# Optimization experiments

Measured on AMD Instinct MI355X. Metric: run time of the kernel, lower is better.

The kernel has to match this reference:

```python
import jax, jax.numpy as jnp
import numpy as np

N_NODES = 50000
N_EDGES = 800000
IN_SIZE, HID_SIZE, OUT_SIZE = 512, 128, 64


def _graph_conv(feat, src, dst, W, b, out_norm, in_norm, activation=None):
    # DGL GraphConv with norm='both': h' = D_in^{-1/2} A D_out^{-1/2} (X W) + b
    x = feat * out_norm[:, None]          # scale by source (out-degree) norm
    x = x @ W                             # dense transform first (in >= out)
    msg = x[src]                          # gather per-edge messages [E, d]
    agg = jax.ops.segment_sum(msg, dst, num_segments=N_NODES)
    h = agg * in_norm[:, None] + b
    if activation is not None:
        h = activation(h)
    return h


def setup_inputs() -> dict:
    key = jax.random.key(0)
    k1, k2, k3, k4, k5, k6, k7 = jax.random.split(key, 7)
    features = jax.random.normal(k1, (N_NODES, IN_SIZE), dtype=jnp.float32)
    src = jax.random.randint(k2, (N_EDGES,), 0, N_NODES, dtype=jnp.int64)
    dst = jax.random.randint(k3, (N_EDGES,), 0, N_NODES, dtype=jnp.int64)
    # Glorot-style init as in dglnn.GraphConv
    W1 = jax.random.normal(k4, (IN_SIZE, HID_SIZE), dtype=jnp.float32) * (1.0 / np.sqrt(IN_SIZE))
    b1 = jnp.zeros((HID_SIZE,), dtype=jnp.float32)
    W2 = jax.random.normal(k5, (HID_SIZE, OUT_SIZE), dtype=jnp.float32) * (1.0 / np.sqrt(HID_SIZE))
    b2 = jnp.zeros((OUT_SIZE,), dtype=jnp.float32)
    return {"features": features, "W1": W1, "b1": b1, "W2": W2, "b2": b2,
            "src": src, "dst": dst}


def reference(features, W1, b1, W2, b2, src, dst):
    ones = jnp.ones((N_EDGES,), dtype=features.dtype)
    out_deg = jax.ops.segment_sum(ones, src, num_segments=N_NODES)
    in_deg = jax.ops.segment_sum(ones, dst, num_segments=N_NODES)
    out_norm = jax.lax.rsqrt(jnp.clip(out_deg, 1.0))  # deg clamped to >=1 as in DGL
    in_norm = jax.lax.rsqrt(jnp.clip(in_deg, 1.0))
    h = _graph_conv(features, src, dst, W1, b1, out_norm, in_norm, activation=jax.nn.relu)
    # dropout omitted (eval mode)
    h = _graph_conv(h, src, dst, W2, b2, out_norm, in_norm, activation=None)
    return h
```

## Files before the change

### kernel.cpp

```cpp
#include <hip/hip_runtime.h>

#define N_NODES 50000
#define IN_SIZE 512
#define HID 128
#define OUT 64
#define NB 256
#define SHIFT 7
#define NBUCK 391
#define SB 64
#define NBINS32 25000

typedef _Float16 f16x8 __attribute__((ext_vector_type(8)));
typedef _Float16 f16x2 __attribute__((ext_vector_type(2)));
typedef float    f32x4 __attribute__((ext_vector_type(4)));

__device__ __forceinline__ bool detect_w(const int* p, int t, int* sh) {
    if (t < 64) {
        unsigned long long m = __ballot(p[2 * t + 1] == 0);
        if (t == 0) *sh = (m == ~0ull) ? 1 : 0;
    }
    __syncthreads();
    return *sh != 0;
}

__device__ __forceinline__ int load_idx(const void* p, int e, bool w) {
    return w ? (int)((const long long*)p)[e] : ((const int*)p)[e];
}

__global__ __launch_bounds__(256) void k_chist_wt(const void* __restrict__ dstp,
                                                  int* __restrict__ hist, int E, int EPB,
                                                  const float* __restrict__ W1, _Float16* __restrict__ W1T,
                                                  const float* __restrict__ W2, _Float16* __restrict__ W2T) {
    const int t = threadIdx.x, b = blockIdx.x;
    if (b >= NB) {
        int i = (b - NB) * 256 + t;
        if (i < IN_SIZE * HID) {
            int k = i >> 7, n = i & (HID - 1);
            W1T[(size_t)n * IN_SIZE + k] = (_Float16)W1[i];
        } else {
            int j = i - IN_SIZE * HID;
            if (j < HID * OUT) {
                int k = j >> 6, n = j & (OUT - 1);
                W2T[(size_t)n * HID + k] = (_Float16)W2[j];
            }
        }
        return;
    }
    __shared__ int bins[NBUCK];
    __shared__ int shw;
    for (int i = t; i < NBUCK; i += 256) bins[i] = 0;
    bool w = detect_w((const int*)dstp, t, &shw);
    __syncthreads();
    int eend = min(E, (b + 1) * EPB);
    for (int e = b * EPB + t; e < eend; e += 256)
        atomicAdd(&bins[load_idx(dstp, e, w) >> SHIFT], 1);
    __syncthreads();
    for (int i = t; i < NBUCK; i += 256) hist[i * NB + b] = bins[i];
}

__global__ __launch_bounds__(256) void k_srchist(const void* __restrict__ srcp,
                                                 unsigned int* __restrict__ partial, int E, int ESB) {
    __shared__ unsigned int bins[NBINS32];
    __shared__ int shw;
    const int t = threadIdx.x, b = blockIdx.x;
    for (int i = t; i < NBINS32; i += 256) bins[i] = 0;
    bool w = detect_w((const int*)srcp, t, &shw);
    __syncthreads();
    int eend = min(E, (b + 1) * ESB);
    for (int e = b * ESB + t; e < eend; e += 256) {
        int s = load_idx(srcp, e, w);
        atomicAdd(&bins[s >> 1], 1u << ((s & 1) << 4));
    }
    __syncthreads();
    for (int i = t; i < NBINS32; i += 256) partial[(size_t)b * NBINS32 + i] = bins[i];
}

__global__ __launch_bounds__(256) void k_sred(const unsigned int* __restrict__ partial,
                                              float* __restrict__ onorm) {
    int wd = blockIdx.x * 256 + threadIdx.x;
    if (wd >= NBINS32) return;
    int c0 = 0, c1 = 0;
    for (int b = 0; b < SB; ++b) {
        unsigned int v = partial[(size_t)b * NBINS32 + wd];
        c0 += (int)(v & 0xFFFFu);
        c1 += (int)(v >> 16);
    }
    if (c0 < 1) c0 = 1;
    if (c1 < 1) c1 = 1;
    onorm[2 * wd]     = 1.0f / sqrtf((float)c0);
    onorm[2 * wd + 1] = 1.0f / sqrtf((float)c1);
}

__global__ __launch_bounds__(256) void k_scanA(int* __restrict__ hist, int* __restrict__ bsum) {
    __shared__ int s[256];
    const int t = threadIdx.x, g = blockIdx.x;
    int v = hist[g * NB + t];
    s[t] = v;
    __syncthreads();
    for (int off = 1; off < 256; off <<= 1) {
        int u = (t >= off) ? s[t - off] : 0;
        __syncthreads();
        s[t] += u;
        __syncthreads();
    }
    hist[g * NB + t] = s[t] - v;
    if (t == 255) bsum[g] = s[255];
}

__global__ __launch_bounds__(512) void k_scanB(const int* __restrict__ bsum, int* __restrict__ bb) {
    __shared__ int s[512];
    const int t = threadIdx.x;
    int v = (t < NBUCK) ? bsum[t] : 0;
    s[t] = v;
    __syncthreads();
    for (int off = 1; off < 512; off <<= 1) {
        int u = (t >= off) ? s[t - off] : 0;
        __syncthreads();
        s[t] += u;
        __syncthreads();
    }
    if (t <= NBUCK) bb[t] = s[t] - v;
}

__global__ __launch_bounds__(256) void k_cscatter(const void* __restrict__ srcp,
                                                  const void* __restrict__ dstp,
                                                  const int* __restrict__ hist,
                                                  const int* __restrict__ bb,
                                                  int* __restrict__ tmp_src,
                                                  unsigned char* __restrict__ tmp_dl,
                                                  int E, int EPB) {
    __shared__ int cur[NBUCK];
    __shared__ int shw;
    const int t = threadIdx.x, b = blockIdx.x;
    for (int i = t; i < NBUCK; i += 256) cur[i] = hist[i * NB + b] + bb[i];
    bool w = detect_w((const int*)dstp, t, &shw);
    __syncthreads();
    int eend = min(E, (b + 1) * EPB);
    for (int e = b * EPB + t; e < eend; e += 256) {
        int s = load_idx(srcp, e, w);
        int d = load_idx(dstp, e, w);
        int pos = atomicAdd(&cur[d >> SHIFT], 1);
        tmp_src[pos] = s;
        tmp_dl[pos]  = (unsigned char)(d & 127);
    }
}

__global__ __launch_bounds__(256) void k_fine(const int* __restrict__ tmp_src,
                                              const unsigned char* __restrict__ tmp_dl,
                                              const int* __restrict__ bb,
                                              int* __restrict__ rp,
                                              int* __restrict__ esrc,
                                              float* __restrict__ innorm) {
    __shared__ int fcnt[128];
    __shared__ int sc[128];
    __shared__ int fcur[128];
    const int t = threadIdx.x, u = blockIdx.x;
    const int e0 = bb[u], e1 = bb[u + 1];
    if (t < 128) fcnt[t] = 0;
    __syncthreads();
    for (int e = e0 + t; e < e1; e += 256)
        atomicAdd(&fcnt[tmp_dl[e]], 1);
    __syncthreads();
    if (t < 128) sc[t] = fcnt[t];
    __syncthreads();
    for (int off = 1; off < 128; off <<= 1) {
        int v = (t < 128 && t >= off) ? sc[t - off] : 0;
        __syncthreads();
        if (t < 128) sc[t] += v;
        __syncthreads();
    }
    if (t < 128) {
        int base = e0 + sc[t] - fcnt[t];
        fcur[t] = base;
        int node = u * 128 + t;
        if (node < N_NODES) {
            rp[node] = base;
            int c = fcnt[t]; if (c < 1) c = 1;
            innorm[node] = 1.0f / sqrtf((float)c);
        }
    }
    if (u == NBUCK - 1 && t == 0) rp[N_NODES] = e1;
    __syncthreads();
    for (int e = e0 + t; e < e1; e += 256) {
        int pos = atomicAdd(&fcur[tmp_dl[e]], 1);
        esrc[pos] = tmp_src[e];
    }
}

#define LDA 40
__global__ __launch_bounds__(256) void k_gemm1_mfma(const float* __restrict__ A,
                                                    const _Float16* __restrict__ BT,
                                                    const float* __restrict__ onorm,
                                                    _Float16* __restrict__ X) {
    __shared__ _Float16 As[64 * LDA];
    __shared__ _Float16 Bs[128 * LDA];
    const int tid  = threadIdx.x;
    const int wave = tid >> 6, lane = tid & 63;
    const int lm = lane & 15, lq = lane >> 4;
    const int row0 = blockIdx.x * 64;

    const int ar = tid >> 2, aq = tid & 3;
    int arow = row0 + ar; if (arow >= N_NODES) arow = N_NODES - 1;
    const float* aptr = A + (size_t)arow * IN_SIZE + aq * 8;
    _Float16* asd = &As[ar * LDA + aq * 8];
    const int bn = tid >> 1, bh = tid & 1;
    const _Float16* bptr = BT + (size_t)bn * IN_SIZE + bh * 16;
    _Float16* bsd = &Bs[bn * LDA + bh * 16];

    f32x4 acc[8];
#pragma unroll
    for (int nt = 0; nt < 8; ++nt) acc[nt] = (f32x4){0.f, 0.f, 0.f, 0.f};

    for (int k0 = 0; k0 < IN_SIZE; k0 += 32) {
        float4 a0 = *(const float4*)(aptr + k0);
        float4 a1 = *(const float4*)(aptr + k0 + 4);
        f16x8  b0 = *(const f16x8*)(bptr + k0);
        f16x8  b1 = *(const f16x8*)(bptr + k0 + 8);
        f16x8 ap = {(_Float16)a0.x, (_Float16)a0.y, (_Float16)a0.z, (_Float16)a0.w,
                    (_Float16)a1.x, (_Float16)a1.y, (_Float16)a1.z, (_Float16)a1.w};
        __syncthreads();
        *(f16x8*)asd       = ap;
        *(f16x8*)bsd       = b0;
        *(f16x8*)(bsd + 8) = b1;
        __syncthreads();
        f16x8 af = *(const f16x8*)&As[(wave * 16 + lm) * LDA + lq * 8];
#pragma unroll
        for (int nt = 0; nt < 8; ++nt) {
            f16x8 bf = *(const f16x8*)&Bs[(nt * 16 + lm) * LDA + lq * 8];
            acc[nt] = __builtin_amdgcn_mfma_f32_16x16x32_f16(af, bf, acc[nt], 0, 0, 0);
        }
    }
#pragma unroll
    for (int i = 0; i < 4; ++i) {
        int row = row0 + wave * 16 + lq * 4 + i;
        if (row < N_NODES) {
            float on = onorm[row];
            _Float16* o = X + (size_t)row * HID + lm;
#pragma unroll
            for (int nt = 0; nt < 8; ++nt)
                o[nt * 16] = (_Float16)(acc[nt][i] * on);
        }
    }
}

__global__ __launch_bounds__(256) void k_agg1(const _Float16* __restrict__ X, const int* __restrict__ rp,
                                              const int* __restrict__ esrc, const float* __restrict__ innorm,
                                              const float* __restrict__ onorm, const float* __restrict__ b1,
                                              _Float16* __restrict__ H) {
    const int n = blockIdx.x * 4 + (threadIdx.x >> 6);
    const int c = (threadIdx.x & 63) << 1;
    if (n >= N_NODES) return;
    const int e0 = rp[n], e1 = rp[n + 1];
    float a0 = 0.f, a1 = 0.f;
    int e = e0;
    for (; e + 3 < e1; e += 4) {
        int s0 = esrc[e], s1 = esrc[e + 1], s2 = esrc[e + 2], s3 = esrc[e + 3];
        f16x2 v0 = *(const f16x2*)&X[(size_t)s0 * HID + c];
        f16x2 v1 = *(const f16x2*)&X[(size_t)s1 * HID + c];
        f16x2 v2 = *(const f16x2*)&X[(size_t)s2 * HID + c];
        f16x2 v3 = *(const f16x2*)&X[(size_t)s3 * HID + c];
        a0 += ((float)v0.x + (float)v1.x) + ((float)v2.x + (float)v3.x);
        a1 += ((float)v0.y + (float)v1.y) + ((float)v2.y + (float)v3.y);
    }
    for (; e < e1; ++e) {
        f16x2 v = *(const f16x2*)&X[(size_t)esrc[e] * HID + c];
        a0 += (float)v.x; a1 += (float)v.y;
    }
    float inn = innorm[n], on = onorm[n];
    float2 b = *(const float2*)&b1[c];
    float h0 = fmaxf(a0 * inn + b.x, 0.f) * on;
    float h1 = fmaxf(a1 * inn + b.y, 0.f) * on;
    *(f16x2*)&H[(size_t)n * HID + c] = (f16x2){(_Float16)h0, (_Float16)h1};
}

#define LDK 136
__global__ __launch_bounds__(256) void k_gemm2_mfma(const _Float16* __restrict__ Hm,
                                                    const _Float16* __restrict__ W2T,
                                                    _Float16* __restrict__ X2) {
    __shared__ _Float16 Hs[64 * LDK];
    __shared__ _Float16 Ws[64 * LDK];
    const int tid  = threadIdx.x;
    const int wave = tid >> 6, lane = tid & 63;
    const int lm = lane & 15, lq = lane >> 4;
    const int row0 = blockIdx.x * 64;

    const int r = tid >> 2, cch = (tid & 3) * 32;
    int hrow = row0 + r; if (hrow >= N_NODES) hrow = N_NODES - 1;
    const _Float16* hp = Hm + (size_t)hrow * HID + cch;
    const _Float16* wp = W2T + (size_t)r * HID + cch;
    _Float16* hd = &Hs[r * LDK + cch];
    _Float16* wd = &Ws[r * LDK + cch];
#pragma unroll
    for (int i = 0; i < 4; ++i) {
        *(f16x8*)(hd + i * 8) = *(const f16x8*)(hp + i * 8);
        *(f16x8*)(wd + i * 8) = *(const f16x8*)(wp + i * 8);
    }
    __syncthreads();

    f32x4 acc[4];
#pragma unroll
    for (int nt = 0; nt < 4; ++nt) acc[nt] = (f32x4){0.f, 0.f, 0.f, 0.f};
#pragma unroll
    for (int k0 = 0; k0 < HID; k0 += 32) {
        f16x8 af = *(const f16x8*)&Hs[(wave * 16 + lm) * LDK + k0 + lq * 8];
#pragma unroll
        for (int nt = 0; nt < 4; ++nt) {
            f16x8 bf = *(const f16x8*)&Ws[(nt * 16 + lm) * LDK + k0 + lq * 8];
            acc[nt] = __builtin_amdgcn_mfma_f32_16x16x32_f16(af, bf, acc[nt], 0, 0, 0);
        }
    }
#pragma unroll
    for (int i = 0; i < 4; ++i) {
        int row = row0 + wave * 16 + lq * 4 + i;
        if (row < N_NODES) {
            _Float16* o = X2 + (size_t)row * OUT + lm;
#pragma unroll
            for (int nt = 0; nt < 4; ++nt)
                o[nt * 16] = (_Float16)acc[nt][i];
        }
    }
}

__global__ __launch_bounds__(256) void k_agg2(const _Float16* __restrict__ X2, const int* __restrict__ rp,
                                              const int* __restrict__ esrc, const float* __restrict__ innorm,
                                              const float* __restrict__ b2, float* __restrict__ out) {
    const int n = blockIdx.x * 8 + (threadIdx.x >> 5);
    const int c = (threadIdx.x & 31) << 1;
    if (n >= N_NODES) return;
    const int e0 = rp[n], e1 = rp[n + 1];
    float a0 = 0.f, a1 = 0.f;
    int e = e0;
    for (; e + 3 < e1; e += 4) {
        int s0 = esrc[e], s1 = esrc[e + 1], s2 = esrc[e + 2], s3 = esrc[e + 3];
        f16x2 v0 = *(const f16x2*)&X2[(size_t)s0 * OUT + c];
        f16x2 v1 = *(const f16x2*)&X2[(size_t)s1 * OUT + c];
        f16x2 v2 = *(const f16x2*)&X2[(size_t)s2 * OUT + c];
        f16x2 v3 = *(const f16x2*)&X2[(size_t)s3 * OUT + c];
        a0 += ((float)v0.x + (float)v1.x) + ((float)v2.x + (float)v3.x);
        a1 += ((float)v0.y + (float)v1.y) + ((float)v2.y + (float)v3.y);
    }
    for (; e < e1; ++e) {
        f16x2 v = *(const f16x2*)&X2[(size_t)esrc[e] * OUT + c];
        a0 += (float)v.x; a1 += (float)v.y;
    }
    float inn = innorm[n];
    float2 b = *(const float2*)&b2[c];
    *(float2*)&out[(size_t)n * OUT + c] = make_float2(a0 * inn + b.x, a1 * inn + b.y);
}

extern "C" void kernel_launch(void* const* d_in, const int* in_sizes, int n_in,
                              void* d_out, int out_size, void* d_ws, size_t ws_size,
                              hipStream_t stream) {
    const float* feat = (const float*)d_in[0];
    const float* W1   = (const float*)d_in[1];
    const float* b1   = (const float*)d_in[2];
    const float* W2   = (const float*)d_in[3];
    const float* b2   = (const float*)d_in[4];
    const void*  srcp = (const void*)d_in[5];
    const void*  dstp = (const void*)d_in[6];
    const int    E    = in_sizes[5];
    float* out = (float*)d_out;

    char* w = (char*)d_ws;
    size_t off = 0;
    auto alloc = [&](size_t bytes) -> void* {
        off = (off + 255) & ~(size_t)255;
        void* p = w + off;
        off += bytes;
        return p;
    };
    int*   hist    = (int*)alloc((size_t)NBUCK * NB * 4);
    int*   bsum    = (int*)alloc((size_t)NBUCK * 4);
    int*   bb      = (int*)alloc((size_t)(NBUCK + 1) * 4);
    int*   rp      = (int*)alloc((size_t)(N_NODES + 1) * 4);
    unsigned int* spart = (unsigned int*)alloc((size_t)SB * NBINS32 * 4);
    int*   tmp_src = (int*)alloc((size_t)E * 4);
    unsigned char* tmp_dl = (unsigned char*)alloc((size_t)E);
    int*   esrc    = (int*)alloc((size_t)E * 4);
    float* onorm   = (float*)alloc((size_t)N_NODES * 4);
    float* innorm  = (float*)alloc((size_t)N_NODES * 4);
    _Float16* W1T  = (_Float16*)alloc((size_t)IN_SIZE * HID * 2);
    _Float16* W2T  = (_Float16*)alloc((size_t)HID * OUT * 2);
    _Float16* X1   = (_Float16*)alloc((size_t)N_NODES * HID * 2);
    _Float16* Hbuf = (_Float16*)alloc((size_t)N_NODES * HID * 2);
    _Float16* X2   = (_Float16*)alloc((size_t)N_NODES * OUT * 2);
    (void)ws_size; (void)n_in; (void)out_size;

    const int EPB = (E + NB - 1) / NB;
    const int ESB = (E + SB - 1) / SB;
    const int WTB = (IN_SIZE * HID + HID * OUT + 255) / 256;

    k_chist_wt<<<NB + WTB, 256, 0, stream>>>(dstp, hist, E, EPB, W1, W1T, W2, W2T);
    k_srchist<<<SB, 256, 0, stream>>>(srcp, spart, E, ESB);
    k_sred<<<(NBINS32 + 255) / 256, 256, 0, stream>>>(spart, onorm);
    k_scanA<<<NBUCK, 256, 0, stream>>>(hist, bsum);
    k_scanB<<<1, 512, 0, stream>>>(bsum, bb);
    k_cscatter<<<NB, 256, 0, stream>>>(srcp, dstp, hist, bb, tmp_src, tmp_dl, E, EPB);
    k_fine<<<NBUCK, 256, 0, stream>>>(tmp_src, tmp_dl, bb, rp, esrc, innorm);

    k_gemm1_mfma<<<(N_NODES + 63) / 64, 256, 0, stream>>>(feat, W1T, onorm, X1);
    k_agg1<<<(N_NODES + 3) / 4, 256, 0, stream>>>(X1, rp, esrc, innorm, onorm, b1, Hbuf);
    k_gemm2_mfma<<<(N_NODES + 63) / 64, 256, 0, stream>>>(Hbuf, W2T, X2);
    k_agg2<<<(N_NODES + 7) / 8, 256, 0, stream>>>(X2, rp, esrc, innorm, b2, out);
}
```

Baseline: 316.6 us.

## Fuse agg1 into gemm2, fold source-degree reduction into k_fine, pack scatter temp

The layer-1 neighbor aggregation now runs inside the layer-2 GEMM kernel. Each block aggregates 64 rows straight into LDS, so the fp16 hidden buffer is never written to or read back from global memory. The per-node source-degree reduction moves from a separate kernel into k_fine. The source index and local destination offset are packed into one 32-bit temp array, which cuts a launch and one stream of scattered stores. The cost is that the gather, previously spread over many small blocks, now runs as a sequential 16-row loop per wave with fewer resident blocks. That gives less latency hiding for the random gathers.

After: 341.1 us. 7.7% more time.

```diff
diff --git a/kernel.cpp b/kernel.cpp
--- a/kernel.cpp
+++ b/kernel.cpp
@@ -75,22 +75,6 @@
     for (int i = t; i < NBINS32; i += 256) partial[(size_t)b * NBINS32 + i] = bins[i];
 }
 
-__global__ __launch_bounds__(256) void k_sred(const unsigned int* __restrict__ partial,
-                                              float* __restrict__ onorm) {
-    int wd = blockIdx.x * 256 + threadIdx.x;
-    if (wd >= NBINS32) return;
-    int c0 = 0, c1 = 0;
-    for (int b = 0; b < SB; ++b) {
-        unsigned int v = partial[(size_t)b * NBINS32 + wd];
-        c0 += (int)(v & 0xFFFFu);
-        c1 += (int)(v >> 16);
-    }
-    if (c0 < 1) c0 = 1;
-    if (c1 < 1) c1 = 1;
-    onorm[2 * wd]     = 1.0f / sqrtf((float)c0);
-    onorm[2 * wd + 1] = 1.0f / sqrtf((float)c1);
-}
-
 __global__ __launch_bounds__(256) void k_scanA(int* __restrict__ hist, int* __restrict__ bsum) {
     __shared__ int s[256];
     const int t = threadIdx.x, g = blockIdx.x;
@@ -126,8 +110,7 @@
                                                   const void* __restrict__ dstp,
                                                   const int* __restrict__ hist,
                                                   const int* __restrict__ bb,
-                                                  int* __restrict__ tmp_src,
-                                                  unsigned char* __restrict__ tmp_dl,
+                                                  unsigned int* __restrict__ tmp,
                                                   int E, int EPB) {
     __shared__ int cur[NBUCK];
     __shared__ int shw;
@@ -140,17 +123,17 @@
         int s = load_idx(srcp, e, w);
         int d = load_idx(dstp, e, w);
         int pos = atomicAdd(&cur[d >> SHIFT], 1);
-        tmp_src[pos] = s;
-        tmp_dl[pos]  = (unsigned char)(d & 127);
-    }
-}
-
-__global__ __launch_bounds__(256) void k_fine(const int* __restrict__ tmp_src,
-                                              const unsigned char* __restrict__ tmp_dl,
+        tmp[pos] = (unsigned int)s | ((unsigned int)(d & 127) << 16);
+    }
+}
+
+__global__ __launch_bounds__(256) void k_fine(const unsigned int* __restrict__ tmp,
                                               const int* __restrict__ bb,
+                                              const unsigned int* __restrict__ partial,
                                               int* __restrict__ rp,
                                               int* __restrict__ esrc,
-                                              float* __restrict__ innorm) {
+                                              float* __restrict__ innorm,
+                                              float* __restrict__ onorm) {
     __shared__ int fcnt[128];
     __shared__ int sc[128];
     __shared__ int fcur[128];
@@ -159,7 +142,22 @@
     if (t < 128) fcnt[t] = 0;
     __syncthreads();
     for (int e = e0 + t; e < e1; e += 256)
-        atomicAdd(&fcnt[tmp_dl[e]], 1);
+        atomicAdd(&fcnt[tmp[e] >> 16], 1);
+    if (t < 64) {
+        int wd = u * 64 + t;
+        if (wd < NBINS32) {
+            int c0 = 0, c1 = 0;
+            for (int b = 0; b < SB; ++b) {
+                unsigned int v = partial[(size_t)b * NBINS32 + wd];
+                c0 += (int)(v & 0xFFFFu);
+                c1 += (int)(v >> 16);
+            }
+            if (c0 < 1) c0 = 1;
+            if (c1 < 1) c1 = 1;
+            onorm[2 * wd]     = 1.0f / sqrtf((float)c0);
+            if (2 * wd + 1 < N_NODES) onorm[2 * wd + 1] = 1.0f / sqrtf((float)c1);
+        }
+    }
     __syncthreads();
     if (t < 128) sc[t] = fcnt[t];
     __syncthreads();
@@ -182,8 +180,9 @@
     if (u == NBUCK - 1 && t == 0) rp[N_NODES] = e1;
     __syncthreads();
     for (int e = e0 + t; e < e1; e += 256) {
-        int pos = atomicAdd(&fcur[tmp_dl[e]], 1);
-        esrc[pos] = tmp_src[e];
+        unsigned int p = tmp[e];
+        int pos = atomicAdd(&fcur[p >> 16], 1);
+        esrc[pos] = (int)(p & 0xFFFFu);
     }
 }
 
@@ -243,60 +242,64 @@
     }
 }
 
-__global__ __launch_bounds__(256) void k_agg1(const _Float16* __restrict__ X, const int* __restrict__ rp,
-                                              const int* __restrict__ esrc, const float* __restrict__ innorm,
-                                              const float* __restrict__ onorm, const float* __restrict__ b1,
-                                              _Float16* __restrict__ H) {
-    const int n = blockIdx.x * 4 + (threadIdx.x >> 6);
-    const int c = (threadIdx.x & 63) << 1;
-    if (n >= N_NODES) return;
-    const int e0 = rp[n], e1 = rp[n + 1];
-    float a0 = 0.f, a1 = 0.f;
-    int e = e0;
-    for (; e + 3 < e1; e += 4) {
-        int s0 = esrc[e], s1 = esrc[e + 1], s2 = esrc[e + 2], s3 = esrc[e + 3];
-        f16x2 v0 = *(const f16x2*)&X[(size_t)s0 * HID + c];
-        f16x2 v1 = *(const f16x2*)&X[(size_t)s1 * HID + c];
-        f16x2 v2 = *(const f16x2*)&X[(size_t)s2 * HID + c];
-        f16x2 v3 = *(const f16x2*)&X[(size_t)s3 * HID + c];
-        a0 += ((float)v0.x + (float)v1.x) + ((float)v2.x + (float)v3.x);
-        a1 += ((float)v0.y + (float)v1.y) + ((float)v2.y + (float)v3.y);
-    }
-    for (; e < e1; ++e) {
-        f16x2 v = *(const f16x2*)&X[(size_t)esrc[e] * HID + c];
-        a0 += (float)v.x; a1 += (float)v.y;
-    }
-    float inn = innorm[n], on = onorm[n];
-    float2 b = *(const float2*)&b1[c];
-    float h0 = fmaxf(a0 * inn + b.x, 0.f) * on;
-    float h1 = fmaxf(a1 * inn + b.y, 0.f) * on;
-    *(f16x2*)&H[(size_t)n * HID + c] = (f16x2){(_Float16)h0, (_Float16)h1};
-}
-
 #define LDK 136
-__global__ __launch_bounds__(256) void k_gemm2_mfma(const _Float16* __restrict__ Hm,
+__global__ __launch_bounds__(256) void k_agg1_gemm2(const _Float16* __restrict__ X,
+                                                    const int* __restrict__ rp,
+                                                    const int* __restrict__ esrc,
+                                                    const float* __restrict__ innorm,
+                                                    const float* __restrict__ onorm,
+                                                    const float* __restrict__ b1,
                                                     const _Float16* __restrict__ W2T,
                                                     _Float16* __restrict__ X2) {
     __shared__ _Float16 Hs[64 * LDK];
     __shared__ _Float16 Ws[64 * LDK];
     const int tid  = threadIdx.x;
     const int wave = tid >> 6, lane = tid & 63;
+    const int row0 = blockIdx.x * 64;
+
+    {
+        const int r = tid >> 2, cch = (tid & 3) * 32;
+        const _Float16* wp = W2T + (size_t)r * HID + cch;
+        _Float16* wd = &Ws[r * LDK + cch];
+#pragma unroll
+        for (int i = 0; i < 4; ++i)
+            *(f16x8*)(wd + i * 8) = *(const f16x8*)(wp + i * 8);
+    }
+
+    const int c = lane << 1;
+    float2 b = *(const float2*)&b1[c];
+#pragma unroll 1
+    for (int i = 0; i < 16; ++i) {
+        const int r = wave * 16 + i;
+        const int n = row0 + r;
+        if (n >= N_NODES) {
+            *(f16x2*)&Hs[r * LDK + c] = (f16x2){(_Float16)0.f, (_Float16)0.f};
+            continue;
+        }
+        const int e0 = rp[n], e1 = rp[n + 1];
+        float a0 = 0.f, a1 = 0.f;
+        int e = e0;
+        for (; e + 3 < e1; e += 4) {
+            int s0 = esrc[e], s1 = esrc[e + 1], s2 = esrc[e + 2], s3 = esrc[e + 3];
+            f16x2 v0 = *(const f16x2*)&X[(size_t)s0 * HID + c];
+            f16x2 v1 = *(const f16x2*)&X[(size_t)s1 * HID + c];
+            f16x2 v2 = *(const f16x2*)&X[(size_t)s2 * HID + c];
+            f16x2 v3 = *(const f16x2*)&X[(size_t)s3 * HID + c];
+            a0 += ((float)v0.x + (float)v1.x) + ((float)v2.x + (float)v3.x);
+            a1 += ((float)v0.y + (float)v1.y) + ((float)v2.y + (float)v3.y);
+        }
+        for (; e < e1; ++e) {
+            f16x2 v = *(const f16x2*)&X[(size_t)esrc[e] * HID + c];
+            a0 += (float)v.x; a1 += (float)v.y;
+        }
+        float inn = innorm[n], on = onorm[n];
+        float h0 = fmaxf(a0 * inn + b.x, 0.f) * on;
+        float h1 = fmaxf(a1 * inn + b.y, 0.f) * on;
+        *(f16x2*)&Hs[r * LDK + c] = (f16x2){(_Float16)h0, (_Float16)h1};
+    }
+    __syncthreads();
+
     const int lm = lane & 15, lq = lane >> 4;
-    const int row0 = blockIdx.x * 64;
-
-    const int r = tid >> 2, cch = (tid & 3) * 32;
-    int hrow = row0 + r; if (hrow >= N_NODES) hrow = N_NODES - 1;
-    const _Float16* hp = Hm + (size_t)hrow * HID + cch;
-    const _Float16* wp = W2T + (size_t)r * HID + cch;
-    _Float16* hd = &Hs[r * LDK + cch];
-    _Float16* wd = &Ws[r * LDK + cch];
-#pragma unroll
-    for (int i = 0; i < 4; ++i) {
-        *(f16x8*)(hd + i * 8) = *(const f16x8*)(hp + i * 8);
-        *(f16x8*)(wd + i * 8) = *(const f16x8*)(wp + i * 8);
-    }
-    __syncthreads();
-
     f32x4 acc[4];
 #pragma unroll
     for (int nt = 0; nt < 4; ++nt) acc[nt] = (f32x4){0.f, 0.f, 0.f, 0.f};
@@ -374,15 +377,13 @@
     int*   bb      = (int*)alloc((size_t)(NBUCK + 1) * 4);
     int*   rp      = (int*)alloc((size_t)(N_NODES + 1) * 4);
     unsigned int* spart = (unsigned int*)alloc((size_t)SB * NBINS32 * 4);
-    int*   tmp_src = (int*)alloc((size_t)E * 4);
-    unsigned char* tmp_dl = (unsigned char*)alloc((size_t)E);
+    unsigned int* tmp   = (unsigned int*)alloc((size_t)E * 4);
     int*   esrc    = (int*)alloc((size_t)E * 4);
     float* onorm   = (float*)alloc((size_t)N_NODES * 4);
     float* innorm  = (float*)alloc((size_t)N_NODES * 4);
     _Float16* W1T  = (_Float16*)alloc((size_t)IN_SIZE * HID * 2);
     _Float16* W2T  = (_Float16*)alloc((size_t)HID * OUT * 2);
     _Float16* X1   = (_Float16*)alloc((size_t)N_NODES * HID * 2);
-    _Float16* Hbuf = (_Float16*)alloc((size_t)N_NODES * HID * 2);
     _Float16* X2   = (_Float16*)alloc((size_t)N_NODES * OUT * 2);
     (void)ws_size; (void)n_in; (void)out_size;
 
@@ -392,14 +393,12 @@
 
     k_chist_wt<<<NB + WTB, 256, 0, stream>>>(dstp, hist, E, EPB, W1, W1T, W2, W2T);
     k_srchist<<<SB, 256, 0, stream>>>(srcp, spart, E, ESB);
-    k_sred<<<(NBINS32 + 255) / 256, 256, 0, stream>>>(spart, onorm);
     k_scanA<<<NBUCK, 256, 0, stream>>>(hist, bsum);
     k_scanB<<<1, 512, 0, stream>>>(bsum, bb);
-    k_cscatter<<<NB, 256, 0, stream>>>(srcp, dstp, hist, bb, tmp_src, tmp_dl, E, EPB);
-    k_fine<<<NBUCK, 256, 0, stream>>>(tmp_src, tmp_dl, bb, rp, esrc, innorm);
+    k_cscatter<<<NB, 256, 0, stream>>>(srcp, dstp, hist, bb, tmp, E, EPB);
+    k_fine<<<NBUCK, 256, 0, stream>>>(tmp, bb, spart, rp, esrc, innorm, onorm);
 
     k_gemm1_mfma<<<(N_NODES + 63) / 64, 256, 0, stream>>>(feat, W1T, onorm, X1);
-    k_agg1<<<(N_NODES + 3) / 4, 256, 0, stream>>>(X1, rp, esrc, innorm, onorm, b1, Hbuf);
-    k_gemm2_mfma<<<(N_NODES + 63) / 64, 256, 0, stream>>>(Hbuf, W2T, X2);
+    k_agg1_gemm2<<<(N_NODES + 63) / 64, 256, 0, stream>>>(X1, rp, esrc, innorm, onorm, b1, W2T, X2);
     k_agg2<<<(N_NODES + 7) / 8, 256, 0, stream>>>(X2, rp, esrc, innorm, b2, out);
 }
```
